# Kernel tuning notes

Hardware: AMD Instinct MI355X
Metric: run time of the kernel (lower is better)

Reference implementation:

```python
import jax, jax.numpy as jnp
import numpy as np

B, S, D = 2, 2048, 2048
H = 16
HD = D // H  # 128

def setup_inputs() -> dict:
    key = jax.random.key(0)
    k1, k2, k3 = jax.random.split(key, 3)
    x = jax.random.normal(k1, (B, S, D), dtype=jnp.float32)
    w_qkv = jax.random.normal(k2, (D, 3 * D), dtype=jnp.float32) * (1.0 / np.sqrt(D))
    b_qkv = jnp.zeros((3 * D,), dtype=jnp.float32)
    w_out = jax.random.normal(k3, (D, D), dtype=jnp.float32) * (1.0 / np.sqrt(D))
    b_out = jnp.zeros((D,), dtype=jnp.float32)
    return {"x": x, "w_qkv": w_qkv, "b_qkv": b_qkv, "w_out": w_out, "b_out": b_out}

def reference(x, w_qkv, b_qkv, w_out, b_out):
    batch, seq_len, channels = x.shape
    qkv = x @ w_qkv + b_qkv                      # [B,S,3D]
    q, k, v = jnp.split(qkv, 3, axis=-1)
    # [B,S,D] -> [B,H,S,HD]
    def heads(t):
        return t.reshape(batch, seq_len, H, HD).transpose(0, 2, 1, 3)
    q, k, v = heads(q), heads(k), heads(v)
    scale = 1.0 / np.sqrt(HD).astype(np.float32)
    attn = jnp.einsum('bhqd,bhkd->bhqk', q, k) * scale
    causal = jnp.tril(jnp.ones((seq_len, seq_len), dtype=bool))
    attn = jnp.where(causal, attn, -jnp.inf)
    attn = jax.nn.softmax(attn, axis=-1)
    y = jnp.einsum('bhqk,bhkd->bhqd', attn, v)   # [B,H,S,HD]
    y = y.transpose(0, 2, 1, 3).reshape(batch, seq_len, channels)
    return y @ w_out + b_out
```

## Files before the change

kernel.cpp:

```cpp
#include <hip/hip_runtime.h>
#include <hip/hip_bf16.h>
#include <cstdint>
#include <cstddef>

#define BB 2
#define SS 2048
#define DD 2048
#define HH 16
#define HDIM 128
#define QSCALE 0.12751743f

typedef short bf16x8 __attribute__((ext_vector_type(8)));
typedef float f32x4 __attribute__((ext_vector_type(4)));

__device__ __forceinline__ ushort f2bf(float f) {
    union { float f; uint32_t u; } v; v.f = f;
    uint32_t u = v.u;
    u += 0x7fffu + ((u >> 16) & 1u);
    return (ushort)(u >> 16);
}

__device__ __forceinline__ ushort f2bf_fast(float f) {
    union { float f; uint32_t u; } v; v.f = f;
    return (ushort)((v.u + 0x8000u) >> 16);
}

__device__ __forceinline__ void gl16(const ushort* g, ushort* l) {
    __builtin_amdgcn_global_load_lds(
        (const __attribute__((address_space(1))) unsigned int*)g,
        (__attribute__((address_space(3))) unsigned int*)l,
        16, 0, 0);
}

__global__ __launch_bounds__(256) void cast_x_kernel(
    const float* __restrict__ X, ushort* __restrict__ Xb)
{
    size_t idx = ((size_t)blockIdx.x * 256 + threadIdx.x) * 8;
    float4 a = *(const float4*)(X + idx);
    float4 b = *(const float4*)(X + idx + 4);
    ushort4 o0, o1;
    o0.x = f2bf(a.x); o0.y = f2bf(a.y); o0.z = f2bf(a.z); o0.w = f2bf(a.w);
    o1.x = f2bf(b.x); o1.y = f2bf(b.y); o1.z = f2bf(b.z); o1.w = f2bf(b.w);
    *(ushort4*)(Xb + idx) = o0;
    *(ushort4*)(Xb + idx + 4) = o1;
}

__global__ __launch_bounds__(256) void transpose_cast_kernel(
    const float* __restrict__ W, ushort* __restrict__ Wt, int K, int N)
{
    __shared__ ushort tile[32][36];
    const int n0 = blockIdx.x * 32;
    const int k0 = blockIdx.y * 32;
    const int t = threadIdx.x;
    const int r = t >> 3;
    const int c = (t & 7) * 4;
    float4 a = *(const float4*)(W + (size_t)(k0 + r) * N + n0 + c);
    tile[r][c + 0] = f2bf(a.x); tile[r][c + 1] = f2bf(a.y);
    tile[r][c + 2] = f2bf(a.z); tile[r][c + 3] = f2bf(a.w);
    __syncthreads();
    ushort4 o;
    o.x = tile[c + 0][r]; o.y = tile[c + 1][r];
    o.z = tile[c + 2][r]; o.w = tile[c + 3][r];
    *(ushort4*)(Wt + (size_t)(n0 + r) * K + k0 + c) = o;
}

__global__ __launch_bounds__(256) void transpose_v_kernel(
    const ushort* __restrict__ V, ushort* __restrict__ Vt)
{
    __shared__ ushort tile[32][36];
    const int s0 = blockIdx.x * 32;
    const int h0 = blockIdx.y * 32;
    const int bh = blockIdx.z;
    const ushort* Vp = V + (size_t)bh * SS * HDIM;
    ushort* Vtp = Vt + (size_t)bh * HDIM * SS;
    const int t = threadIdx.x;
    const int r = t >> 3;
    const int c = (t & 7) * 4;
    *(ushort4*)&tile[r][c] = *(const ushort4*)(Vp + (size_t)(s0 + r) * HDIM + h0 + c);
    __syncthreads();
    ushort4 o;
    o.x = tile[c + 0][r]; o.y = tile[c + 1][r];
    o.z = tile[c + 2][r]; o.w = tile[c + 3][r];
    *(ushort4*)(Vtp + (size_t)(h0 + r) * SS + s0 + c) = o;
}

__global__ __launch_bounds__(256) void gemm_qkv_kernel(
    const ushort* __restrict__ A, const ushort* __restrict__ Bt,
    const float* __restrict__ bias,
    ushort* __restrict__ Qo, ushort* __restrict__ Ko, ushort* __restrict__ Vo)
{
    const int n0 = blockIdx.x * 128;
    const int m0 = blockIdx.y * 128;
    __shared__ ushort As[128 * 32];
    __shared__ ushort Bs[128 * 32];
    const int t = threadIdx.x, w = t >> 6, lane = t & 63;
    const int l15 = lane & 15, quad = lane >> 4;
    const int lrow = lane >> 2, lks = lane & 3;
    const int wr = w >> 1, wc = w & 1;

    f32x4 acc[4][4];
#pragma unroll
    for (int i = 0; i < 4; ++i)
#pragma unroll
        for (int j = 0; j < 4; ++j) acc[i][j] = (f32x4){0.f, 0.f, 0.f, 0.f};

    for (int k0 = 0; k0 < DD; k0 += 32) {
        __syncthreads();
#pragma unroll
        for (int q = 0; q < 2; ++q) {
            int e = w * 2 + q;
            int row = e * 16 + lrow;
            gl16(A  + (size_t)(m0 + row) * DD + k0 + lks * 8, &As[e * 512]);
            gl16(Bt + (size_t)(n0 + row) * DD + k0 + lks * 8, &Bs[e * 512]);
        }
        __syncthreads();
        bf16x8 ar[4], br[4];
#pragma unroll
        for (int i = 0; i < 4; ++i)
            ar[i] = *(const bf16x8*)&As[(wr * 64 + i * 16 + l15) * 32 + quad * 8];
#pragma unroll
        for (int j = 0; j < 4; ++j)
            br[j] = *(const bf16x8*)&Bs[(wc * 64 + j * 16 + l15) * 32 + quad * 8];
#pragma unroll
        for (int i = 0; i < 4; ++i)
#pragma unroll
            for (int j = 0; j < 4; ++j)
                acc[i][j] = __builtin_amdgcn_mfma_f32_16x16x32_bf16(ar[i], br[j], acc[i][j], 0, 0, 0);
    }

    const int bidx = m0 >> 11;
#pragma unroll
    for (int j = 0; j < 4; ++j) {
        int n = n0 + wc * 64 + j * 16 + l15;
        int which = n >> 11, c = n & 2047, h = c >> 7, hd = c & 127;
        ushort* dst = (which == 0) ? Qo : ((which == 1) ? Ko : Vo);
        float bv = bias[n];
        float sc = (which == 0) ? QSCALE : 1.0f;
        size_t base = ((size_t)(bidx * HH + h) * SS) * HDIM + hd;
#pragma unroll
        for (int i = 0; i < 4; ++i) {
            int s = (m0 & 2047) + wr * 64 + i * 16 + quad * 4;
#pragma unroll
            for (int r = 0; r < 4; ++r)
                dst[base + (size_t)(s + r) * HDIM] = f2bf((acc[i][j][r] + bv) * sc);
        }
    }
}

__global__ __launch_bounds__(256) void gemm_out_kernel(
    const ushort* __restrict__ A, const ushort* __restrict__ Bt,
    const float* __restrict__ bias, float* __restrict__ Out)
{
    const int n0 = blockIdx.x * 128;
    const int m0 = blockIdx.y * 128;
    __shared__ ushort As[128 * 32];
    __shared__ ushort Bs[128 * 32];
    const int t = threadIdx.x, w = t >> 6, lane = t & 63;
    const int l15 = lane & 15, quad = lane >> 4;
    const int lrow = lane >> 2, lks = lane & 3;
    const int wr = w >> 1, wc = w & 1;

    f32x4 acc[4][4];
#pragma unroll
    for (int i = 0; i < 4; ++i)
#pragma unroll
        for (int j = 0; j < 4; ++j) acc[i][j] = (f32x4){0.f, 0.f, 0.f, 0.f};

    for (int k0 = 0; k0 < DD; k0 += 32) {
        __syncthreads();
#pragma unroll
        for (int q = 0; q < 2; ++q) {
            int e = w * 2 + q;
            int row = e * 16 + lrow;
            gl16(A  + (size_t)(m0 + row) * DD + k0 + lks * 8, &As[e * 512]);
            gl16(Bt + (size_t)(n0 + row) * DD + k0 + lks * 8, &Bs[e * 512]);
        }
        __syncthreads();
        bf16x8 ar[4], br[4];
#pragma unroll
        for (int i = 0; i < 4; ++i)
            ar[i] = *(const bf16x8*)&As[(wr * 64 + i * 16 + l15) * 32 + quad * 8];
#pragma unroll
        for (int j = 0; j < 4; ++j)
            br[j] = *(const bf16x8*)&Bs[(wc * 64 + j * 16 + l15) * 32 + quad * 8];
#pragma unroll
        for (int i = 0; i < 4; ++i)
#pragma unroll
            for (int j = 0; j < 4; ++j)
                acc[i][j] = __builtin_amdgcn_mfma_f32_16x16x32_bf16(ar[i], br[j], acc[i][j], 0, 0, 0);
    }

#pragma unroll
    for (int j = 0; j < 4; ++j) {
        int n = n0 + wc * 64 + j * 16 + l15;
        float bv = bias[n];
#pragma unroll
        for (int i = 0; i < 4; ++i) {
            int m = m0 + wr * 64 + i * 16 + quad * 4;
#pragma unroll
            for (int r = 0; r < 4; ++r)
                Out[(size_t)(m + r) * DD + n] = acc[i][j][r] + bv;
        }
    }
}

__global__ __launch_bounds__(256, 4) void attn_mfma_kernel(
    const ushort* __restrict__ Q, const ushort* __restrict__ K,
    const ushort* __restrict__ Vt, ushort* __restrict__ Y)
{
    const int bh = blockIdx.y;
    const int qt = gridDim.x - 1 - blockIdx.x;
    const int q0 = qt * 64;
    const int b = bh >> 4, h = bh & 15;

    __shared__ ushort Ks[4 * 64 * 32];
    __shared__ ushort Vs[2 * 128 * 32];
    __shared__ ushort Ps[64 * 32];

    const int t = threadIdx.x, w = t >> 6, lane = t & 63;
    const int l15 = lane & 15, quad = lane >> 4;
    const int lrow = lane >> 2, lks = lane & 3;

    const ushort* Qp = Q  + (size_t)bh * SS * HDIM;
    const ushort* Kp = K  + (size_t)bh * SS * HDIM;
    const ushort* Vp = Vt + (size_t)bh * HDIM * SS;

    bf16x8 aq[4];
#pragma unroll
    for (int ks = 0; ks < 4; ++ks)
        aq[ks] = *(const bf16x8*)(Qp + (size_t)(q0 + w * 16 + l15) * HDIM + ks * 32 + quad * 8);

    bf16x8 ones;
#pragma unroll
    for (int j = 0; j < 8; ++j) ones[j] = (short)0x3F80;

    f32x4 O[8];
#pragma unroll
    for (int nt = 0; nt < 8; ++nt) O[nt] = (f32x4){0.f, 0.f, 0.f, 0.f};
    f32x4 Ol = (f32x4){0.f, 0.f, 0.f, 0.f};

    for (int kb = 0; kb <= qt; ++kb) {
        const int kbase = kb * 64;
        __syncthreads();
#pragma unroll
        for (int g = 0; g < 4; ++g) {
            int row = g * 16 + lrow;
            gl16(Kp + (size_t)(kbase + row) * HDIM + w * 32 + lks * 8,
                 &Ks[w * 2048 + g * 512]);
        }
#pragma unroll
        for (int g = 0; g < 4; ++g) {
            int e = w * 4 + g;
            int pan = e >> 3, dg = e & 7;
            int dim = dg * 16 + lrow;
            gl16(Vp + (size_t)dim * SS + kbase + pan * 32 + lks * 8,
                 &Vs[pan * 4096 + dg * 512]);
        }
        __syncthreads();

        f32x4 sc[4];
#pragma unroll
        for (int jt = 0; jt < 4; ++jt) sc[jt] = (f32x4){0.f, 0.f, 0.f, 0.f};
#pragma unroll
        for (int jt = 0; jt < 4; ++jt)
#pragma unroll
            for (int ks = 0; ks < 4; ++ks) {
                bf16x8 bk = *(const bf16x8*)&Ks[ks * 2048 + (jt * 16 + l15) * 32 + quad * 8];
                sc[jt] = __builtin_amdgcn_mfma_f32_16x16x32_bf16(aq[ks], bk, sc[jt], 0, 0, 0);
            }

        if (kb == qt) {
#pragma unroll
            for (int jt = 0; jt < 4; ++jt) {
                int col = jt * 16 + l15;
#pragma unroll
                for (int r = 0; r < 4; ++r) {
                    int row = w * 16 + quad * 4 + r;
                    if (col > row) sc[jt][r] = -1e30f;
                }
            }
        }

#pragma unroll
        for (int hf = 0; hf < 2; ++hf) {
#pragma unroll
            for (int jj = 0; jj < 2; ++jj) {
                int jt = hf * 2 + jj;
                int chunk = jj * 2 + (l15 >> 3);
                int elem  = l15 & 7;
#pragma unroll
                for (int r = 0; r < 4; ++r) {
                    float p = __builtin_amdgcn_exp2f(sc[jt][r]);
                    int row = w * 16 + quad * 4 + r;
                    Ps[row * 32 + ((chunk ^ quad) << 3) + elem] = f2bf_fast(p);
                }
            }
            bf16x8 ap = *(const bf16x8*)&Ps[(w * 16 + l15) * 32 + ((quad ^ (l15 >> 2)) << 3)];
#pragma unroll
            for (int nt = 0; nt < 8; ++nt) {
                bf16x8 bv = *(const bf16x8*)&Vs[hf * 4096 + (nt * 16 + l15) * 32 + quad * 8];
                O[nt] = __builtin_amdgcn_mfma_f32_16x16x32_bf16(ap, bv, O[nt], 0, 0, 0);
            }
            Ol = __builtin_amdgcn_mfma_f32_16x16x32_bf16(ap, ones, Ol, 0, 0, 0);
        }
    }

    f32x4 rl;
#pragma unroll
    for (int r = 0; r < 4; ++r) rl[r] = 1.0f / Ol[r];
#pragma unroll
    for (int nt = 0; nt < 8; ++nt)
#pragma unroll
        for (int r = 0; r < 4; ++r) {
            int s = q0 + w * 16 + quad * 4 + r;
            Y[((size_t)(b * SS + s)) * DD + h * HDIM + nt * 16 + l15] =
                f2bf(O[nt][r] * rl[r]);
        }
}

extern "C" void kernel_launch(void* const* d_in, const int* in_sizes, int n_in,
                              void* d_out, int out_size, void* d_ws, size_t ws_size,
                              hipStream_t stream) {
    const float* x     = (const float*)d_in[0];
    const float* w_qkv = (const float*)d_in[1];
    const float* b_qkv = (const float*)d_in[2];
    const float* w_out = (const float*)d_in[3];
    const float* b_out = (const float*)d_in[4];
    float* out = (float*)d_out;

    ushort* ws  = (ushort*)d_ws;
    ushort* xb  = ws;
    ushort* wtq = xb + 8388608;
    ushort* wto = wtq + 12582912;
    ushort* q   = wto + 4194304;
    ushort* k   = q + 8388608;
    ushort* v   = k + 8388608;
    ushort* vt  = v + 8388608;
    ushort* y   = vt + 8388608;

    cast_x_kernel<<<4096, 256, 0, stream>>>(x, xb);
    transpose_cast_kernel<<<dim3(192, 64), 256, 0, stream>>>(w_qkv, wtq, DD, 3 * DD);
    transpose_cast_kernel<<<dim3(64, 64), 256, 0, stream>>>(w_out, wto, DD, DD);
    gemm_qkv_kernel<<<dim3(48, 32), 256, 0, stream>>>(xb, wtq, b_qkv, q, k, v);
    transpose_v_kernel<<<dim3(64, 4, 32), 256, 0, stream>>>(v, vt);
    attn_mfma_kernel<<<dim3(32, 32), 256, 0, stream>>>(q, k, vt, y);
    gemm_out_kernel<<<dim3(16, 32), 256, 0, stream>>>(y, wto, b_out, out);
}
```

Before: 423.1 us.

## Fuse V transpose into QKV GEMM and retile attention with 32x32 MFMA

```diff
diff --git a/kernel.cpp b/kernel.cpp
--- a/kernel.cpp
+++ b/kernel.cpp
@@ -12,6 +12,7 @@
 
 typedef short bf16x8 __attribute__((ext_vector_type(8)));
 typedef float f32x4 __attribute__((ext_vector_type(4)));
+typedef float f32x16 __attribute__((ext_vector_type(16)));
 
 __device__ __forceinline__ ushort f2bf(float f) {
     union { float f; uint32_t u; } v; v.f = f;
@@ -64,30 +65,10 @@
     *(ushort4*)(Wt + (size_t)(n0 + r) * K + k0 + c) = o;
 }
 
-__global__ __launch_bounds__(256) void transpose_v_kernel(
-    const ushort* __restrict__ V, ushort* __restrict__ Vt)
-{
-    __shared__ ushort tile[32][36];
-    const int s0 = blockIdx.x * 32;
-    const int h0 = blockIdx.y * 32;
-    const int bh = blockIdx.z;
-    const ushort* Vp = V + (size_t)bh * SS * HDIM;
-    ushort* Vtp = Vt + (size_t)bh * HDIM * SS;
-    const int t = threadIdx.x;
-    const int r = t >> 3;
-    const int c = (t & 7) * 4;
-    *(ushort4*)&tile[r][c] = *(const ushort4*)(Vp + (size_t)(s0 + r) * HDIM + h0 + c);
-    __syncthreads();
-    ushort4 o;
-    o.x = tile[c + 0][r]; o.y = tile[c + 1][r];
-    o.z = tile[c + 2][r]; o.w = tile[c + 3][r];
-    *(ushort4*)(Vtp + (size_t)(h0 + r) * SS + s0 + c) = o;
-}
-
 __global__ __launch_bounds__(256) void gemm_qkv_kernel(
     const ushort* __restrict__ A, const ushort* __restrict__ Bt,
     const float* __restrict__ bias,
-    ushort* __restrict__ Qo, ushort* __restrict__ Ko, ushort* __restrict__ Vo)
+    ushort* __restrict__ Qo, ushort* __restrict__ Ko, ushort* __restrict__ Vto)
 {
     const int n0 = blockIdx.x * 128;
     const int m0 = blockIdx.y * 128;
@@ -129,20 +110,35 @@
     }
 
     const int bidx = m0 >> 11;
+    const int which = n0 >> 11;
 #pragma unroll
     for (int j = 0; j < 4; ++j) {
         int n = n0 + wc * 64 + j * 16 + l15;
-        int which = n >> 11, c = n & 2047, h = c >> 7, hd = c & 127;
-        ushort* dst = (which == 0) ? Qo : ((which == 1) ? Ko : Vo);
+        int c = n & 2047, h = c >> 7, hd = c & 127;
         float bv = bias[n];
-        float sc = (which == 0) ? QSCALE : 1.0f;
-        size_t base = ((size_t)(bidx * HH + h) * SS) * HDIM + hd;
-#pragma unroll
-        for (int i = 0; i < 4; ++i) {
-            int s = (m0 & 2047) + wr * 64 + i * 16 + quad * 4;
-#pragma unroll
-            for (int r = 0; r < 4; ++r)
-                dst[base + (size_t)(s + r) * HDIM] = f2bf((acc[i][j][r] + bv) * sc);
+        if (which == 2) {
+            size_t base = ((size_t)(bidx * HH + h) * HDIM + hd) * SS;
+#pragma unroll
+            for (int i = 0; i < 4; ++i) {
+                int s = (m0 & 2047) + wr * 64 + i * 16 + quad * 4;
+                ushort4 pk;
+                pk.x = f2bf(acc[i][j][0] + bv);
+                pk.y = f2bf(acc[i][j][1] + bv);
+                pk.z = f2bf(acc[i][j][2] + bv);
+                pk.w = f2bf(acc[i][j][3] + bv);
+                *(ushort4*)(Vto + base + s) = pk;
+            }
+        } else {
+            ushort* dst = (which == 0) ? Qo : Ko;
+            float sc = (which == 0) ? QSCALE : 1.0f;
+            size_t base = ((size_t)(bidx * HH + h) * SS) * HDIM + hd;
+#pragma unroll
+            for (int i = 0; i < 4; ++i) {
+                int s = (m0 & 2047) + wr * 64 + i * 16 + quad * 4;
+#pragma unroll
+                for (int r = 0; r < 4; ++r)
+                    dst[base + (size_t)(s + r) * HDIM] = f2bf((acc[i][j][r] + bv) * sc);
+            }
         }
     }
 }
@@ -204,118 +200,121 @@
     }
 }
 
-__global__ __launch_bounds__(256, 4) void attn_mfma_kernel(
+__global__ __launch_bounds__(256, 2) void attn_mfma_kernel(
     const ushort* __restrict__ Q, const ushort* __restrict__ K,
     const ushort* __restrict__ Vt, ushort* __restrict__ Y)
 {
     const int bh = blockIdx.y;
     const int qt = gridDim.x - 1 - blockIdx.x;
-    const int q0 = qt * 64;
+    const int q0 = qt * 128;
     const int b = bh >> 4, h = bh & 15;
 
     __shared__ ushort Ks[4 * 64 * 32];
     __shared__ ushort Vs[2 * 128 * 32];
-    __shared__ ushort Ps[64 * 32];
+    __shared__ ushort Ps[128 * 32];
 
     const int t = threadIdx.x, w = t >> 6, lane = t & 63;
-    const int l15 = lane & 15, quad = lane >> 4;
+    const int l31 = lane & 31, hh = lane >> 5;
     const int lrow = lane >> 2, lks = lane & 3;
+    const int sw31 = l31 & 3;
 
     const ushort* Qp = Q  + (size_t)bh * SS * HDIM;
     const ushort* Kp = K  + (size_t)bh * SS * HDIM;
     const ushort* Vp = Vt + (size_t)bh * HDIM * SS;
 
-    bf16x8 aq[4];
-#pragma unroll
-    for (int ks = 0; ks < 4; ++ks)
-        aq[ks] = *(const bf16x8*)(Qp + (size_t)(q0 + w * 16 + l15) * HDIM + ks * 32 + quad * 8);
+    bf16x8 aq[8];
+#pragma unroll
+    for (int kb2 = 0; kb2 < 8; ++kb2)
+        aq[kb2] = *(const bf16x8*)(Qp + (size_t)(q0 + w * 32 + l31) * HDIM + kb2 * 16 + hh * 8);
 
     bf16x8 ones;
 #pragma unroll
     for (int j = 0; j < 8; ++j) ones[j] = (short)0x3F80;
 
-    f32x4 O[8];
-#pragma unroll
-    for (int nt = 0; nt < 8; ++nt) O[nt] = (f32x4){0.f, 0.f, 0.f, 0.f};
-    f32x4 Ol = (f32x4){0.f, 0.f, 0.f, 0.f};
-
-    for (int kb = 0; kb <= qt; ++kb) {
+    f32x16 O[4];
+#pragma unroll
+    for (int nt = 0; nt < 4; ++nt) O[nt] = (f32x16)0.f;
+    f32x16 Ol = (f32x16)0.f;
+
+    const int kbdiag = 2 * qt + (w >> 1);
+    const int nkb = 2 * qt + 2;
+
+    for (int kb = 0; kb < nkb; ++kb) {
         const int kbase = kb * 64;
         __syncthreads();
 #pragma unroll
         for (int g = 0; g < 4; ++g) {
-            int row = g * 16 + lrow;
-            gl16(Kp + (size_t)(kbase + row) * HDIM + w * 32 + lks * 8,
+            int key = g * 16 + lrow;
+            int chunk = lks ^ (key & 3);
+            gl16(Kp + (size_t)(kbase + key) * HDIM + w * 32 + chunk * 8,
                  &Ks[w * 2048 + g * 512]);
         }
 #pragma unroll
         for (int g = 0; g < 4; ++g) {
-            int e = w * 4 + g;
-            int pan = e >> 3, dg = e & 7;
-            int dim = dg * 16 + lrow;
-            gl16(Vp + (size_t)dim * SS + kbase + pan * 32 + lks * 8,
-                 &Vs[pan * 4096 + dg * 512]);
-        }
-        __syncthreads();
-
-        f32x4 sc[4];
-#pragma unroll
-        for (int jt = 0; jt < 4; ++jt) sc[jt] = (f32x4){0.f, 0.f, 0.f, 0.f};
-#pragma unroll
-        for (int jt = 0; jt < 4; ++jt)
-#pragma unroll
-            for (int ks = 0; ks < 4; ++ks) {
-                bf16x8 bk = *(const bf16x8*)&Ks[ks * 2048 + (jt * 16 + l15) * 32 + quad * 8];
-                sc[jt] = __builtin_amdgcn_mfma_f32_16x16x32_bf16(aq[ks], bk, sc[jt], 0, 0, 0);
-            }
-
-        if (kb == qt) {
-#pragma unroll
-            for (int jt = 0; jt < 4; ++jt) {
-                int col = jt * 16 + l15;
-#pragma unroll
-                for (int r = 0; r < 4; ++r) {
-                    int row = w * 16 + quad * 4 + r;
-                    if (col > row) sc[jt][r] = -1e30f;
+            int pan = g >> 1, sub = g & 1;
+            int dim = w * 32 + sub * 16 + lrow;
+            int chunk = lks ^ (dim & 3);
+            gl16(Vp + (size_t)dim * SS + kbase + pan * 32 + chunk * 8,
+                 &Vs[pan * 4096 + (w * 32 + sub * 16) * 32]);
+        }
+        __syncthreads();
+
+        const bool active = (kb <= kbdiag);
+        if (active) {
+            f32x16 sc0 = (f32x16)0.f, sc1 = (f32x16)0.f;
+#pragma unroll
+            for (int kb2 = 0; kb2 < 8; ++kb2) {
+                int c = (kb2 & 1) * 2 + hh;
+                int co = ((c ^ sw31) * 8);
+                bf16x8 bk0 = *(const bf16x8*)&Ks[(kb2 >> 1) * 2048 + l31 * 32 + co];
+                bf16x8 bk1 = *(const bf16x8*)&Ks[(kb2 >> 1) * 2048 + (32 + l31) * 32 + co];
+                sc0 = __builtin_amdgcn_mfma_f32_32x32x16_bf16(aq[kb2], bk0, sc0, 0, 0, 0);
+                sc1 = __builtin_amdgcn_mfma_f32_32x32x16_bf16(aq[kb2], bk1, sc1, 0, 0, 0);
+            }
+
+            if (kb == kbdiag) {
+#pragma unroll
+                for (int r = 0; r < 16; ++r) {
+                    int rowg = q0 + w * 32 + (r & 3) + 8 * (r >> 2) + 4 * hh;
+                    if (kbase + l31 > rowg)      sc0[r] = -1e30f;
+                    if (kbase + 32 + l31 > rowg) sc1[r] = -1e30f;
                 }
             }
-        }
-
-#pragma unroll
-        for (int hf = 0; hf < 2; ++hf) {
-#pragma unroll
-            for (int jj = 0; jj < 2; ++jj) {
-                int jt = hf * 2 + jj;
-                int chunk = jj * 2 + (l15 >> 3);
-                int elem  = l15 & 7;
-#pragma unroll
-                for (int r = 0; r < 4; ++r) {
-                    float p = __builtin_amdgcn_exp2f(sc[jt][r]);
-                    int row = w * 16 + quad * 4 + r;
-                    Ps[row * 32 + ((chunk ^ quad) << 3) + elem] = f2bf_fast(p);
+
+#pragma unroll
+            for (int half = 0; half < 2; ++half) {
+#pragma unroll
+                for (int r = 0; r < 16; ++r) {
+                    float sv = (half == 0) ? sc0[r] : sc1[r];
+                    float p = __builtin_amdgcn_exp2f(sv);
+                    int row = w * 32 + (r & 3) + 8 * (r >> 2) + 4 * hh;
+                    Ps[row * 32 + (((l31 >> 3) ^ (r & 3)) << 3) + (l31 & 7)] = f2bf_fast(p);
                 }
-            }
-            bf16x8 ap = *(const bf16x8*)&Ps[(w * 16 + l15) * 32 + ((quad ^ (l15 >> 2)) << 3)];
-#pragma unroll
-            for (int nt = 0; nt < 8; ++nt) {
-                bf16x8 bv = *(const bf16x8*)&Vs[hf * 4096 + (nt * 16 + l15) * 32 + quad * 8];
-                O[nt] = __builtin_amdgcn_mfma_f32_16x16x32_bf16(ap, bv, O[nt], 0, 0, 0);
-            }
-            Ol = __builtin_amdgcn_mfma_f32_16x16x32_bf16(ap, ones, Ol, 0, 0, 0);
-        }
-    }
-
-    f32x4 rl;
-#pragma unroll
-    for (int r = 0; r < 4; ++r) rl[r] = 1.0f / Ol[r];
-#pragma unroll
-    for (int nt = 0; nt < 8; ++nt)
-#pragma unroll
-        for (int r = 0; r < 4; ++r) {
-            int s = q0 + w * 16 + quad * 4 + r;
-            Y[((size_t)(b * SS + s)) * DD + h * HDIM + nt * 16 + l15] =
-                f2bf(O[nt][r] * rl[r]);
-        }
+#pragma unroll
+                for (int kblk2 = 0; kblk2 < 2; ++kblk2) {
+                    int c = kblk2 * 2 + hh;
+                    int co = ((c ^ sw31) * 8);
+                    bf16x8 ap = *(const bf16x8*)&Ps[(w * 32 + l31) * 32 + co];
+#pragma unroll
+                    for (int nt = 0; nt < 4; ++nt) {
+                        bf16x8 bv = *(const bf16x8*)&Vs[half * 4096 + (nt * 32 + l31) * 32 + co];
+                        O[nt] = __builtin_amdgcn_mfma_f32_32x32x16_bf16(ap, bv, O[nt], 0, 0, 0);
+                    }
+                    Ol = __builtin_amdgcn_mfma_f32_32x32x16_bf16(ap, ones, Ol, 0, 0, 0);
+                }
+            }
+        }
+    }
+
+#pragma unroll
+    for (int r = 0; r < 16; ++r) {
+        int s = q0 + w * 32 + (r & 3) + 8 * (r >> 2) + 4 * hh;
+        float inv = 1.0f / Ol[r];
+        size_t base = ((size_t)(b * SS + s)) * DD + h * HDIM;
+#pragma unroll
+        for (int nt = 0; nt < 4; ++nt)
+            Y[base + nt * 32 + l31] = f2bf(O[nt][r] * inv);
+    }
 }
 
 extern "C" void kernel_launch(void* const* d_in, const int* in_sizes, int n_in,
@@ -334,15 +333,13 @@
     ushort* wto = wtq + 12582912;
     ushort* q   = wto + 4194304;
     ushort* k   = q + 8388608;
-    ushort* v   = k + 8388608;
-    ushort* vt  = v + 8388608;
+    ushort* vt  = k + 8388608;
     ushort* y   = vt + 8388608;
 
     cast_x_kernel<<<4096, 256, 0, stream>>>(x, xb);
     transpose_cast_kernel<<<dim3(192, 64), 256, 0, stream>>>(w_qkv, wtq, DD, 3 * DD);
     transpose_cast_kernel<<<dim3(64, 64), 256, 0, stream>>>(w_out, wto, DD, DD);
-    gemm_qkv_kernel<<<dim3(48, 32), 256, 0, stream>>>(xb, wtq, b_qkv, q, k, v);
-    transpose_v_kernel<<<dim3(64, 4, 32), 256, 0, stream>>>(v, vt);
-    attn_mfma_kernel<<<dim3(32, 32), 256, 0, stream>>>(q, k, vt, y);
+    gemm_qkv_kernel<<<dim3(48, 32), 256, 0, stream>>>(xb, wtq, b_qkv, q, k, vt);
+    attn_mfma_kernel<<<dim3(16, 32), 256, 0, stream>>>(q, k, vt, y);
     gemm_out_kernel<<<dim3(16, 32), 256, 0, stream>>>(y, wto, b_out, out);
 }
```

Measured after the change: 425.8 us. About the same (+0.6%).
